# Kernel tuning notes

Hardware: AMD Instinct MI355X
Metric: run time of the kernel (lower is better)

The kernel has to match this reference:

```python
import jax, jax.numpy as jnp
import numpy as np

B, F, H, D, K = 16384, 4096, 512, 64, 512  # batch, feat, hidden, emb_dim, codebook size
M = H // D  # code positions per sample


def _leaky(h):
    return jnp.where(h > 0, h, 0.01 * h)


def setup_inputs() -> dict:
    key = jax.random.key(0)
    ks = jax.random.split(key, 16)
    lin = lambda k, i, o: jax.random.normal(k, (i, o), jnp.float32) * (1.0 / np.sqrt(i))
    return {
        "x": jax.random.uniform(ks[0], (B, F), jnp.float32),
        "We1": lin(ks[1], F, 256), "be1": jnp.zeros((256,), jnp.float32),
        "We2": lin(ks[2], 256, 128), "be2": jnp.zeros((128,), jnp.float32),
        "We3": lin(ks[3], 128, H), "be3": jnp.zeros((H,), jnp.float32),
        "Wd1": lin(ks[4], H, 128), "bd1": jnp.zeros((128,), jnp.float32),
        "Wd2": lin(ks[5], 128, 256), "bd2": jnp.zeros((256,), jnp.float32),
        "Wd3": lin(ks[6], 256, F), "bd3": jnp.zeros((F,), jnp.float32),
        "codebook": jax.random.normal(ks[7], (D, K), jnp.float32) * 0.02,  # (emb_dim, num_embeddings)
    }


def _nearest(z_e, codebook):
    # z_e: (B, D, M); codebook: (D, K). Squared-distance argmin over K.
    x2 = jnp.sum(z_e * z_e, axis=1)                       # (B, M)
    xw = jnp.einsum('bdm,dk->bmk', z_e, codebook)         # (B, M, K)
    w2 = jnp.sum(codebook * codebook, axis=0)             # (K,)
    idx = jnp.argmin(x2[..., None] - 2.0 * xw + w2, axis=-1)  # (B, M)
    quant = jnp.swapaxes(codebook.T[idx], 1, 2)           # (B, D, M)
    return quant, idx


def reference(x, We1, be1, We2, be2, We3, be3, Wd1, bd1, Wd2, bd2, Wd3, bd3, codebook):
    # encoder MLP
    h = _leaky(x @ We1 + be1)
    h = _leaky(h @ We2 + be2)
    h = _leaky(h @ We3 + be3)                             # (B, H)
    z_e = h.reshape(B, D, M)
    # emb(z_e, weight_sg=True): straight-through, weight detached
    quant_sg, idx = _nearest(z_e, jax.lax.stop_gradient(codebook))
    z_q = z_e + jax.lax.stop_gradient(quant_sg - z_e)
    # emb(z_e.detach()): grads (if any) flow to codebook via gather
    emb, _ = _nearest(jax.lax.stop_gradient(z_e), codebook)
    # decoder MLP
    g = _leaky(z_q.reshape(B, H) @ Wd1 + bd1)
    g = _leaky(g @ Wd2 + bd2)
    X_pred = jax.nn.sigmoid(g @ Wd3 + bd3)                # (B, F)
    return idx, z_e, z_q, emb, X_pred
```

## Files before the change

kernel.cpp:

```cpp
#include <hip/hip_runtime.h>
#include <cstdint>
#include <cstddef>


static constexpr int BB = 16384;

typedef __attribute__((ext_vector_type(8))) short short8;
typedef __attribute__((ext_vector_type(8))) _Float16 half8;
typedef __attribute__((ext_vector_type(4))) float f32x4;

__device__ __forceinline__ unsigned short f2bf(float f) {
    union { float f; uint32_t u; } v; v.f = f;
    uint32_t r = (v.u + 0x7FFFu + ((v.u >> 16) & 1u)) >> 16;
    return (unsigned short)r;
}

__device__ __forceinline__ void lds_barrier() {
    asm volatile("s_waitcnt lgkmcnt(0)" ::: "memory");
    __builtin_amdgcn_s_barrier();
    __builtin_amdgcn_sched_barrier(0);
}

__global__ __launch_bounds__(256) void combine_act(
    const float* __restrict__ part, int S, size_t MN,
    const float* __restrict__ bias, int N,
    float* __restrict__ outF)
{
    const size_t e = ((size_t)blockIdx.x * 256 + threadIdx.x) * 4;
    if (e >= MN) return;
    float4 s = *(const float4*)(part + e);
    for (int i = 1; i < S; i++) {
        const float4 p = *(const float4*)(part + (size_t)i * MN + e);
        s.x += p.x; s.y += p.y; s.z += p.z; s.w += p.w;
    }
    const int col = (int)(e & (size_t)(N - 1));
    const float4 bv = *(const float4*)(bias + col);
    float v0 = s.x + bv.x, v1 = s.y + bv.y, v2 = s.z + bv.z, v3 = s.w + bv.w;
    v0 = (v0 > 0.f) ? v0 : 0.01f * v0;
    v1 = (v1 > 0.f) ? v1 : 0.01f * v1;
    v2 = (v2 > 0.f) ? v2 : 0.01f * v2;
    v3 = (v3 > 0.f) ? v3 : 0.01f * v3;
    float4 o; o.x = v0; o.y = v1; o.z = v2; o.w = v3;
    *(float4*)(outF + e) = o;
}

__global__ __launch_bounds__(256) void transpose_cast(
    const float* __restrict__ W, unsigned short* __restrict__ WT, int R, int Cc)
{
    __shared__ float s[32][33];
    const int tx = threadIdx.x & 31, ty = threadIdx.x >> 5;
    const int c0 = blockIdx.x * 32, r0 = blockIdx.y * 32;
#pragma unroll
    for (int i = 0; i < 4; i++)
        s[ty + i * 8][tx] = W[(size_t)(r0 + ty + i * 8) * Cc + c0 + tx];
    __syncthreads();
#pragma unroll
    for (int i = 0; i < 4; i++)
        WT[(size_t)(c0 + ty + i * 8) * R + r0 + tx] = f2bf(s[tx][ty + i * 8]);
}

__global__ __launch_bounds__(256) void transpose_split_f16(
    const float* __restrict__ W, unsigned short* __restrict__ Th,
    unsigned short* __restrict__ Tl, int R, int Cc)
{
    __shared__ float s[32][33];
    const int tx = threadIdx.x & 31, ty = threadIdx.x >> 5;
    const int c0 = blockIdx.x * 32, r0 = blockIdx.y * 32;
#pragma unroll
    for (int i = 0; i < 4; i++)
        s[ty + i * 8][tx] = W[(size_t)(r0 + ty + i * 8) * Cc + c0 + tx];
    __syncthreads();
#pragma unroll
    for (int i = 0; i < 4; i++) {
        const float f = s[tx][ty + i * 8];
        const _Float16 h = (_Float16)f;
        const float fh = (float)h;
        const _Float16 lo = (_Float16)((f - fh) * 4096.0f);
        union { _Float16 hf; unsigned short u; } ch, cl;
        ch.hf = h; cl.hf = lo;
        Th[(size_t)(c0 + ty + i * 8) * R + r0 + tx] = ch.u;
        Tl[(size_t)(c0 + ty + i * 8) * R + r0 + tx] = cl.u;
    }
}

__global__ __launch_bounds__(512) void cb_w2(
    const float* __restrict__ cb, float* __restrict__ w2g)
{
    const int k = threadIdx.x;
    float s = 0.f;
    for (int d = 0; d < 64; d++) { float c = cb[d * 512 + k]; s = fmaf(c, c, s); }
    w2g[k] = s;
}

template<int BUF>
__device__ __forceinline__ void enc1_step(
    int K0,
    const float* __restrict__ gA,
    const unsigned short* __restrict__ gBh,
    const unsigned short* __restrict__ gBl,
    short (&Ah)[2][2048], short (&Al)[2][2048],
    half8 (&bhC)[4], half8 (&bhN)[4], half8 (&blS)[4],
    f32x4& p0, f32x4& p1,
    f32x4 (&acc1)[4][4], f32x4 (&acc2)[4][4],
    int aoff, int fr0)
{
    constexpr size_t rstep = (size_t)16 * 4096;
    const int kn1 = K0 + 32, kn2 = K0 + 64;
    lds_barrier();
#pragma unroll
    for (int j = 0; j < 4; j++)
        blS[j] = *(const half8*)(gBl + (size_t)j * rstep + K0);
    if (kn1 < 2048) {
#pragma unroll
        for (int j = 0; j < 4; j++)
            bhN[j] = *(const half8*)(gBh + (size_t)j * rstep + kn1);
    }
    f32x4 f0, f1;
    if (kn2 < 2048) {
        f0 = __builtin_nontemporal_load((const f32x4*)(gA + kn2));
        f1 = __builtin_nontemporal_load((const f32x4*)(gA + kn2 + 4));
    }
    half8 ah[4];
#pragma unroll
    for (int i = 0; i < 4; i++)
        ah[i] = *(const half8*)&Ah[BUF][(i << 9) + fr0];
#pragma unroll
    for (int i = 0; i < 4; i++)
#pragma unroll
        for (int j = 0; j < 4; j++)
            acc1[i][j] = __builtin_amdgcn_mfma_f32_16x16x32_f16(
                ah[i], bhC[j], acc1[i][j], 0, 0, 0);
#pragma unroll
    for (int i = 0; i < 4; i++)
#pragma unroll
        for (int j = 0; j < 4; j++)
            acc2[i][j] = __builtin_amdgcn_mfma_f32_16x16x32_f16(
                ah[i], blS[j], acc2[i][j], 0, 0, 0);
    half8 al[4];
#pragma unroll
    for (int i = 0; i < 4; i++)
        al[i] = *(const half8*)&Al[BUF][(i << 9) + fr0];
#pragma unroll
    for (int i = 0; i < 4; i++)
#pragma unroll
        for (int j = 0; j < 4; j++)
            acc2[i][j] = __builtin_amdgcn_mfma_f32_16x16x32_f16(
                al[i], bhC[j], acc2[i][j], 0, 0, 0);
    if (kn1 < 2048) {
        float fv[8];
        *(f32x4*)&fv[0] = p0;
        *(f32x4*)&fv[4] = p1;
        union { _Float16 h[8]; short8 s; } uh, ul;
#pragma unroll
        for (int e = 0; e < 8; e++) {
            const float f = fv[e];
            const _Float16 h = (_Float16)f;
            const float fh = (float)h;
            uh.h[e] = h;
            ul.h[e] = (_Float16)((f - fh) * 4096.0f);
        }
        *(short8*)&Ah[BUF ^ 1][aoff] = uh.s;
        *(short8*)&Al[BUF ^ 1][aoff] = ul.s;
    }
    if (kn2 < 2048) { p0 = f0; p1 = f1; }
}

__global__ __launch_bounds__(256, 2) void gemm_f16x2_enc1(
    const float* __restrict__ X,
    const unsigned short* __restrict__ Bh,
    const unsigned short* __restrict__ Bl,
    float* __restrict__ part)
{
    __shared__ short Ah[2][2048];
    __shared__ short Al[2][2048];
    const int tid = threadIdx.x;
    const int l = tid & 63, w = tid >> 6;
    const int lm = l & 15, lq = l >> 4;
    const int bm = blockIdx.y * 64;
    const int kStart = blockIdx.z * 2048;

    const float* gA = X + (size_t)(bm + w * 16 + lm) * 4096 + kStart + lq * 8;
    const unsigned short* gBh = Bh + (size_t)(w * 64 + lm) * 4096 + kStart + lq * 8;
    const unsigned short* gBl = Bl + (size_t)(w * 64 + lm) * 4096 + kStart + lq * 8;
    constexpr size_t rstep = (size_t)16 * 4096;

    const int aoff = (w << 9) + (l << 3);
    const int fr0 = (lq << 7) + (lm << 3);

    f32x4 acc1[4][4], acc2[4][4];
#pragma unroll
    for (int i = 0; i < 4; i++)
#pragma unroll
        for (int j = 0; j < 4; j++) {
            acc1[i][j] = (f32x4){0.f, 0.f, 0.f, 0.f};
            acc2[i][j] = (f32x4){0.f, 0.f, 0.f, 0.f};
        }

    half8 bhA[4], bhB[4], blS[4];
    f32x4 p0, p1;

    {
#pragma unroll
        for (int j = 0; j < 4; j++)
            bhA[j] = *(const half8*)(gBh + (size_t)j * rstep);
        f32x4 a0 = __builtin_nontemporal_load((const f32x4*)(gA));
        f32x4 a1 = __builtin_nontemporal_load((const f32x4*)(gA + 4));
        p0 = __builtin_nontemporal_load((const f32x4*)(gA + 32));
        p1 = __builtin_nontemporal_load((const f32x4*)(gA + 36));
        float fv[8];
        *(f32x4*)&fv[0] = a0;
        *(f32x4*)&fv[4] = a1;
        union { _Float16 h[8]; short8 s; } uh, ul;
#pragma unroll
        for (int e = 0; e < 8; e++) {
            const float f = fv[e];
            const _Float16 h = (_Float16)f;
            const float fh = (float)h;
            uh.h[e] = h;
            ul.h[e] = (_Float16)((f - fh) * 4096.0f);
        }
        *(short8*)&Ah[0][aoff] = uh.s;
        *(short8*)&Al[0][aoff] = ul.s;
    }

    for (int k2 = 0; k2 < 2048; k2 += 64) {
        enc1_step<0>(k2,      gA, gBh, gBl, Ah, Al, bhA, bhB, blS,
                     p0, p1, acc1, acc2, aoff, fr0);
        enc1_step<1>(k2 + 32, gA, gBh, gBl, Ah, Al, bhB, bhA, blS,
                     p0, p1, acc1, acc2, aoff, fr0);
    }

    float* P = part + (size_t)blockIdx.z * BB * 256;
    const float inv = 0.000244140625f;
#pragma unroll
    for (int i = 0; i < 4; i++)
#pragma unroll
        for (int j = 0; j < 4; j++) {
            const int col = w * 64 + j * 16 + lm;
#pragma unroll
            for (int r = 0; r < 4; r++) {
                const int row = bm + i * 16 + lq * 4 + r;
                P[(size_t)row * 256 + col] = acc1[i][j][r] + inv * acc2[i][j][r];
            }
        }
}

template<int BUF, int NJ, int KLEN>
__device__ __forceinline__ void mid_step(
    int K0,
    const float* __restrict__ gA,
    const unsigned short* __restrict__ gBh,
    const unsigned short* __restrict__ gBl,
    short (&Ah)[2][2048], short (&Al)[2][2048],
    half8 (&bhC)[NJ], half8 (&bhN)[NJ], half8 (&blS)[NJ],
    f32x4& p0, f32x4& p1,
    f32x4 (&acc1)[4][NJ], f32x4 (&acc2)[4][NJ],
    int aoff, int fr0)
{
    constexpr size_t rstep = (size_t)16 * KLEN;
    const int kn1 = K0 + 32, kn2 = K0 + 64;
    lds_barrier();
#pragma unroll
    for (int j = 0; j < NJ; j++)
        blS[j] = *(const half8*)(gBl + (size_t)j * rstep + K0);
    if (kn1 < KLEN) {
#pragma unroll
        for (int j = 0; j < NJ; j++)
            bhN[j] = *(const half8*)(gBh + (size_t)j * rstep + kn1);
    }
    f32x4 f0, f1;
    if (kn2 < KLEN) {
        f0 = *(const f32x4*)(gA + kn2);
        f1 = *(const f32x4*)(gA + kn2 + 4);
    }
    half8 ah[4];
#pragma unroll
    for (int i = 0; i < 4; i++)
        ah[i] = *(const half8*)&Ah[BUF][(i << 9) + fr0];
#pragma unroll
    for (int i = 0; i < 4; i++)
#pragma unroll
        for (int j = 0; j < NJ; j++)
            acc1[i][j] = __builtin_amdgcn_mfma_f32_16x16x32_f16(
                ah[i], bhC[j], acc1[i][j], 0, 0, 0);
#pragma unroll
    for (int i = 0; i < 4; i++)
#pragma unroll
        for (int j = 0; j < NJ; j++)
            acc2[i][j] = __builtin_amdgcn_mfma_f32_16x16x32_f16(
                ah[i], blS[j], acc2[i][j], 0, 0, 0);
    half8 al[4];
#pragma unroll
    for (int i = 0; i < 4; i++)
        al[i] = *(const half8*)&Al[BUF][(i << 9) + fr0];
#pragma unroll
    for (int i = 0; i < 4; i++)
#pragma unroll
        for (int j = 0; j < NJ; j++)
            acc2[i][j] = __builtin_amdgcn_mfma_f32_16x16x32_f16(
                al[i], bhC[j], acc2[i][j], 0, 0, 0);
    if (kn1 < KLEN) {
        float fv[8];
        *(f32x4*)&fv[0] = p0;
        *(f32x4*)&fv[4] = p1;
        union { _Float16 h[8]; short8 s; } uh, ul;
#pragma unroll
        for (int e = 0; e < 8; e++) {
            const float f = fv[e];
            const _Float16 h = (_Float16)f;
            const float fh = (float)h;
            uh.h[e] = h;
            ul.h[e] = (_Float16)((f - fh) * 4096.0f);
        }
        *(short8*)&Ah[BUF ^ 1][aoff] = uh.s;
        *(short8*)&Al[BUF ^ 1][aoff] = ul.s;
    }
    if (kn2 < KLEN) { p0 = f0; p1 = f1; }
}

template<int NJ, int KLEN, int ACT>
__global__ __launch_bounds__(256, 2) void gemm_f16x2_mid(
    const float* __restrict__ A,
    const unsigned short* __restrict__ Bh,
    const unsigned short* __restrict__ Bl,
    const float* __restrict__ bias,
    float* __restrict__ Cf, unsigned short* __restrict__ Cb)
{
    __shared__ short Ah[2][2048];
    __shared__ short Al[2][2048];
    const int tid = threadIdx.x;
    const int l = tid & 63, w = tid >> 6;
    const int lm = l & 15, lq = l >> 4;
    const int bm = blockIdx.y * 64;
    const int bn = blockIdx.x * (64 * NJ);
    const int N = gridDim.x * 64 * NJ;

    const float* gA = A + (size_t)(bm + w * 16 + lm) * KLEN + lq * 8;
    const unsigned short* gBh = Bh + (size_t)(bn + w * (16 * NJ) + lm) * KLEN + lq * 8;
    const unsigned short* gBl = Bl + (size_t)(bn + w * (16 * NJ) + lm) * KLEN + lq * 8;
    constexpr size_t rstep = (size_t)16 * KLEN;

    const int aoff = (w << 9) + (l << 3);
    const int fr0 = (lq << 7) + (lm << 3);

    f32x4 acc1[4][NJ], acc2[4][NJ];
#pragma unroll
    for (int i = 0; i < 4; i++)
#pragma unroll
        for (int j = 0; j < NJ; j++) {
            acc1[i][j] = (f32x4){0.f, 0.f, 0.f, 0.f};
            acc2[i][j] = (f32x4){0.f, 0.f, 0.f, 0.f};
        }

    half8 bhA[NJ], bhB[NJ], blS[NJ];
    f32x4 p0, p1;

    {
#pragma unroll
        for (int j = 0; j < NJ; j++)
            bhA[j] = *(const half8*)(gBh + (size_t)j * rstep);
        f32x4 a0 = *(const f32x4*)(gA);
        f32x4 a1 = *(const f32x4*)(gA + 4);
        p0 = *(const f32x4*)(gA + 32);
        p1 = *(const f32x4*)(gA + 36);
        float fv[8];
        *(f32x4*)&fv[0] = a0;
        *(f32x4*)&fv[4] = a1;
        union { _Float16 h[8]; short8 s; } uh, ul;
#pragma unroll
        for (int e = 0; e < 8; e++) {
            const float f = fv[e];
            const _Float16 h = (_Float16)f;
            const float fh = (float)h;
            uh.h[e] = h;
            ul.h[e] = (_Float16)((f - fh) * 4096.0f);
        }
        *(short8*)&Ah[0][aoff] = uh.s;
        *(short8*)&Al[0][aoff] = ul.s;
    }

    for (int k2 = 0; k2 < KLEN; k2 += 64) {
        mid_step<0, NJ, KLEN>(k2,      gA, gBh, gBl, Ah, Al, bhA, bhB, blS,
                              p0, p1, acc1, acc2, aoff, fr0);
        mid_step<1, NJ, KLEN>(k2 + 32, gA, gBh, gBl, Ah, Al, bhB, bhA, blS,
                              p0, p1, acc1, acc2, aoff, fr0);
    }

    const float inv = 0.000244140625f;
#pragma unroll
    for (int i = 0; i < 4; i++)
#pragma unroll
        for (int j = 0; j < NJ; j++) {
            const int col = bn + w * (16 * NJ) + j * 16 + lm;
            const float bv = bias[col];
#pragma unroll
            for (int r = 0; r < 4; r++) {
                const int row = bm + i * 16 + lq * 4 + r;
                float v = acc1[i][j][r] + inv * acc2[i][j][r] + bv;
                v = (v > 0.f) ? v : 0.01f * v;
                if (ACT == 0) Cf[(size_t)row * N + col] = v;
                else          Cb[(size_t)row * N + col] = f2bf(v);
            }
        }
}

__device__ __forceinline__ void dec3_step(
    int kn,
    const unsigned short* __restrict__ gA,
    const unsigned short* __restrict__ gB,
    short8 (&afC)[4], short8 (&bfC)[4],
    short8 (&afN)[4], short8 (&bfN)[4],
    f32x4 (&acc)[4][4])
{
    if (kn < 256) {
#pragma unroll
        for (int i = 0; i < 4; i++)
            afN[i] = *(const short8*)(gA + (size_t)i * 16 * 256 + kn);
#pragma unroll
        for (int j = 0; j < 4; j++)
            bfN[j] = *(const short8*)(gB + (size_t)j * 16 * 256 + kn);
    }
#pragma unroll
    for (int i = 0; i < 4; i++)
#pragma unroll
        for (int j = 0; j < 4; j++)
            acc[i][j] = __builtin_amdgcn_mfma_f32_16x16x32_bf16(
                afC[i], bfC[j], acc[i][j], 0, 0, 0);
}

__global__ __launch_bounds__(256) void gemm_bf16_dec3(
    const unsigned short* __restrict__ Ag,
    const unsigned short* __restrict__ Bt,
    const float* __restrict__ bias, float* __restrict__ C)
{
    const int tid = threadIdx.x;
    const int l = tid & 63, w = tid >> 6;
    const int lm = l & 15, lq = l >> 4;
    const int bm = blockIdx.y * 128, bn = blockIdx.x * 128;
    const int wm = (w >> 1) * 64, wn = (w & 1) * 64;

    const unsigned short* gA = Ag + (size_t)(bm + wm + lm) * 256 + lq * 8;
    const unsigned short* gB = Bt + (size_t)(bn + wn + lm) * 256 + lq * 8;

    f32x4 acc[4][4];
#pragma unroll
    for (int i = 0; i < 4; i++)
#pragma unroll
        for (int j = 0; j < 4; j++) acc[i][j] = (f32x4){0.f, 0.f, 0.f, 0.f};

    short8 afA[4], afB[4], bfA[4], bfB[4];
#pragma unroll
    for (int i = 0; i < 4; i++)
        afA[i] = *(const short8*)(gA + (size_t)i * 16 * 256);
#pragma unroll
    for (int j = 0; j < 4; j++)
        bfA[j] = *(const short8*)(gB + (size_t)j * 16 * 256);

    for (int k0 = 0; k0 < 256; k0 += 64) {
        dec3_step(k0 + 32, gA, gB, afA, bfA, afB, bfB, acc);
        dec3_step(k0 + 64, gA, gB, afB, bfB, afA, bfA, acc);
    }

#pragma unroll
    for (int i = 0; i < 4; i++) {
#pragma unroll
        for (int j = 0; j < 4; j++) {
            const int col = bn + wn + j * 16 + lm;
            const float bv = bias[col];
#pragma unroll
            for (int r = 0; r < 4; r++) {
                const int row = bm + wm + i * 16 + lq * 4 + r;
                float v = acc[i][j][r] + bv;
                v = 1.0f / (1.0f + __expf(-v));
                C[(size_t)row * 4096 + col] = v;
            }
        }
    }
}

__global__ __launch_bounds__(256) void vq_mfma(
    const float* __restrict__ ze, const float* __restrict__ cb,
    const unsigned short* __restrict__ cbTh,
    const unsigned short* __restrict__ cbTl,
    const float* __restrict__ w2g,
    float* __restrict__ idxf, float* __restrict__ zq, float* __restrict__ emb)
{
    __shared__ short Ahh[2048], All[2048];
    __shared__ float As[64][33];
    __shared__ float redv[32][4];
    __shared__ int   redk[32][4];
    __shared__ int   kq[32];
    const int tid = threadIdx.x;
    const int l = tid & 63, w = tid >> 6;
    const int lm = l & 15, lq = l >> 4;
    const int b0 = blockIdx.x * 4;

    const unsigned short* gBh = cbTh + (size_t)(w * 128 + lm) * 64 + lq * 8;
    const unsigned short* gBl = cbTl + (size_t)(w * 128 + lm) * 64 + lq * 8;
    half8 bh[8], bl[8];
#pragma unroll
    for (int j = 0; j < 8; j++) {
        bh[j] = *(const half8*)(gBh + (size_t)j * 1024);
        bl[j] = *(const half8*)(gBl + (size_t)j * 1024);
    }

#pragma unroll
    for (int ff = 0; ff < 2; ff++) {
        const int e = (tid + ff * 256) * 4;
        const int s = e >> 9, r = e & 511, d = r >> 3, m = r & 7;
        const f32x4 v = *(const f32x4*)(ze + (size_t)b0 * 512 + e);
#pragma unroll
        for (int c = 0; c < 4; c++) {
            const float fv = v[c];
            const int row = s * 8 + m + c;
            As[d][row] = fv;
            const _Float16 h = (_Float16)fv;
            const float fh = (float)h;
            const _Float16 lo = (_Float16)((fv - fh) * 4096.0f);
            union { _Float16 hf; unsigned short u; } ch, cl;
            ch.hf = h; cl.hf = lo;
            const int off = (row >> 4) * 1024 + (d >> 5) * 512 +
                            ((d >> 3) & 3) * 128 + (row & 15) * 8 + (d & 7);
            Ahh[off] = (short)ch.u;
            All[off] = (short)cl.u;
        }
    }
    __syncthreads();

    f32x4 acc1[2][8], acc2[2][8];
#pragma unroll
    for (int i = 0; i < 2; i++)
#pragma unroll
        for (int j = 0; j < 8; j++) {
            acc1[i][j] = (f32x4){0.f, 0.f, 0.f, 0.f};
            acc2[i][j] = (f32x4){0.f, 0.f, 0.f, 0.f};
        }

    const int fr0 = lq * 128 + lm * 8;
    half8 ah0[2], al0[2];
#pragma unroll
    for (int i = 0; i < 2; i++) {
        ah0[i] = *(const half8*)&Ahh[i * 1024 + fr0];
        al0[i] = *(const half8*)&All[i * 1024 + fr0];
    }
#pragma unroll
    for (int i = 0; i < 2; i++)
#pragma unroll
        for (int j = 0; j < 8; j++)
            acc1[i][j] = __builtin_amdgcn_mfma_f32_16x16x32_f16(
                ah0[i], bh[j], acc1[i][j], 0, 0, 0);
#pragma unroll
    for (int i = 0; i < 2; i++)
#pragma unroll
        for (int j = 0; j < 8; j++)
            acc2[i][j] = __builtin_amdgcn_mfma_f32_16x16x32_f16(
                al0[i], bh[j], acc2[i][j], 0, 0, 0);
#pragma unroll
    for (int j = 0; j < 8; j++) {
        half8 nb = *(const half8*)(gBh + (size_t)j * 1024 + 32);
#pragma unroll
        for (int i = 0; i < 2; i++)
            acc2[i][j] = __builtin_amdgcn_mfma_f32_16x16x32_f16(
                ah0[i], bl[j], acc2[i][j], 0, 0, 0);
        bh[j] = nb;
    }
#pragma unroll
    for (int j = 0; j < 8; j++)
        bl[j] = *(const half8*)(gBl + (size_t)j * 1024 + 32);
    half8 ah1[2], al1[2];
#pragma unroll
    for (int i = 0; i < 2; i++) {
        ah1[i] = *(const half8*)&Ahh[i * 1024 + 512 + fr0];
        al1[i] = *(const half8*)&All[i * 1024 + 512 + fr0];
    }
#pragma unroll
    for (int i = 0; i < 2; i++)
#pragma unroll
        for (int j = 0; j < 8; j++)
            acc1[i][j] = __builtin_amdgcn_mfma_f32_16x16x32_f16(
                ah1[i], bh[j], acc1[i][j], 0, 0, 0);
#pragma unroll
    for (int i = 0; i < 2; i++)
#pragma unroll
        for (int j = 0; j < 8; j++)
            acc2[i][j] = __builtin_amdgcn_mfma_f32_16x16x32_f16(
                ah1[i], bl[j], acc2[i][j], 0, 0, 0);
#pragma unroll
    for (int i = 0; i < 2; i++)
#pragma unroll
        for (int j = 0; j < 8; j++)
            acc2[i][j] = __builtin_amdgcn_mfma_f32_16x16x32_f16(
                al1[i], bh[j], acc2[i][j], 0, 0, 0);

    const float inv = 0.000244140625f;
    float w2v[8];
#pragma unroll
    for (int j = 0; j < 8; j++) w2v[j] = w2g[w * 128 + j * 16 + lm];

#pragma unroll
    for (int i = 0; i < 2; i++)
#pragma unroll
        for (int r = 0; r < 4; r++) {
            float bd = 3.4e38f; int bk = 1 << 30;
#pragma unroll
            for (int j = 0; j < 8; j++) {
                const float s = acc1[i][j][r] + inv * acc2[i][j][r];
                const float dsc = w2v[j] - 2.0f * s;
                const int kc = w * 128 + j * 16 + lm;
                if (dsc < bd || (dsc == bd && kc < bk)) { bd = dsc; bk = kc; }
            }
#pragma unroll
            for (int off = 1; off < 16; off <<= 1) {
                const float od = __shfl_xor(bd, off);
                const int   ok = __shfl_xor(bk, off);
                if (od < bd || (od == bd && ok < bk)) { bd = od; bk = ok; }
            }
            if (lm == 0) {
                const int row = i * 16 + lq * 4 + r;
                redv[row][w] = bd;
                redk[row][w] = bk;
            }
        }
    __syncthreads();

    if (tid < 32) {
        float bd = redv[tid][0]; int bk = redk[tid][0];
#pragma unroll
        for (int ww = 1; ww < 4; ww++) {
            const float od = redv[tid][ww];
            const int   ok = redk[tid][ww];
            if (od < bd || (od == bd && ok < bk)) { bd = od; bk = ok; }
        }
        idxf[(size_t)b0 * 8 + tid] = (float)bk;
        kq[tid] = bk;
    }
    __syncthreads();

    {
        const int ss = tid >> 6, dd = tid & 63;
        float zq8[8], em8[8];
#pragma unroll
        for (int mm = 0; mm < 8; mm++) {
            const int k = kq[ss * 8 + mm];
            const float q = cb[dd * 512 + k];
            const float z = As[dd][ss * 8 + mm];
            em8[mm] = q;
            zq8[mm] = z + (q - z);
        }
        float* zqp = zq + (size_t)(b0 + ss) * 512 + dd * 8;
        float* emp = emb + (size_t)(b0 + ss) * 512 + dd * 8;
        *(float4*)zqp = *(float4*)&zq8[0];
        *(float4*)(zqp + 4) = *(float4*)&zq8[4];
        *(float4*)emp = *(float4*)&em8[0];
        *(float4*)(emp + 4) = *(float4*)&em8[4];
    }
}

extern "C" void kernel_launch(void* const* d_in, const int* in_sizes, int n_in,
                              void* d_out, int out_size, void* d_ws, size_t ws_size,
                              hipStream_t stream)
{
    const float* x   = (const float*)d_in[0];
    const float* We1 = (const float*)d_in[1];
    const float* be1 = (const float*)d_in[2];
    const float* We2 = (const float*)d_in[3];
    const float* be2 = (const float*)d_in[4];
    const float* We3 = (const float*)d_in[5];
    const float* be3 = (const float*)d_in[6];
    const float* Wd1 = (const float*)d_in[7];
    const float* bd1 = (const float*)d_in[8];
    const float* Wd2 = (const float*)d_in[9];
    const float* bd2 = (const float*)d_in[10];
    const float* Wd3 = (const float*)d_in[11];
    const float* bd3 = (const float*)d_in[12];
    const float* cb  = (const float*)d_in[13];

    float* out   = (float*)d_out;
    float* o_idx = out;
    float* o_ze  = o_idx + 131072;
    float* o_zq  = o_ze + 8388608;
    float* o_emb = o_zq + 8388608;
    float* o_X   = o_emb + 8388608;

    float* h1 = (float*)d_ws;
    float* h2 = h1 + (size_t)BB * 256;
    float* g1 = h1;
    unsigned short* g2b = (unsigned short*)(h1 + (size_t)BB * 128);
    unsigned short* WT  = (unsigned short*)h2;

    unsigned short* Bth  = (unsigned short*)(o_X + 16777216);
    unsigned short* Btl  = Bth + 1048576;
    unsigned short* W2h  = Btl + 1048576;
    unsigned short* W2l  = W2h + 32768;
    unsigned short* W3h  = W2l + 32768;
    unsigned short* W3l  = W3h + 65536;
    unsigned short* Wd1h = W3l + 65536;
    unsigned short* Wd1l = Wd1h + 65536;
    unsigned short* Wd2h = Wd1l + 65536;
    unsigned short* Wd2l = Wd2h + 32768;
    unsigned short* cbTh = Wd2l + 32768;
    unsigned short* cbTl = cbTh + 32768;
    float*          w2g  = (float*)(cbTl + 32768);

    transpose_split_f16<<<dim3(8, 128), 256, 0, stream>>>(We1, Bth, Btl, 4096, 256);
    transpose_split_f16<<<dim3(4, 8),   256, 0, stream>>>(We2, W2h, W2l, 256, 128);
    transpose_split_f16<<<dim3(16, 4),  256, 0, stream>>>(We3, W3h, W3l, 128, 512);
    transpose_split_f16<<<dim3(4, 16),  256, 0, stream>>>(Wd1, Wd1h, Wd1l, 512, 128);
    transpose_split_f16<<<dim3(8, 4),   256, 0, stream>>>(Wd2, Wd2h, Wd2l, 128, 256);
    transpose_split_f16<<<dim3(16, 2),  256, 0, stream>>>(cb, cbTh, cbTl, 64, 512);
    cb_w2<<<dim3(1), dim3(512), 0, stream>>>(cb, w2g);

    gemm_f16x2_enc1<<<dim3(1, 256, 2), 256, 0, stream>>>(x, Bth, Btl, o_X);
    combine_act<<<4096, 256, 0, stream>>>(o_X, 2, (size_t)BB * 256, be1, 256, h1);
    gemm_f16x2_mid<2, 256, 0><<<dim3(1, 256), 256, 0, stream>>>(
        h1, W2h, W2l, be2, h2, nullptr);
    gemm_f16x2_mid<4, 128, 0><<<dim3(2, 256), 256, 0, stream>>>(
        h2, W3h, W3l, be3, o_ze, nullptr);

    transpose_cast<<<dim3(128, 8), 256, 0, stream>>>(Wd3, WT, 256, 4096);

    vq_mfma<<<dim3(4096), dim3(256), 0, stream>>>(
        o_ze, cb, cbTh, cbTl, w2g, o_idx, o_zq, o_emb);

    gemm_f16x2_mid<2, 512, 0><<<dim3(1, 256), 256, 0, stream>>>(
        o_zq, Wd1h, Wd1l, bd1, g1, nullptr);
    gemm_f16x2_mid<4, 128, 1><<<dim3(1, 256), 256, 0, stream>>>(
        g1, Wd2h, Wd2l, bd2, nullptr, g2b);
    gemm_bf16_dec3<<<dim3(32, 128), 256, 0, stream>>>(g2b, WT, bd3, o_X);
}
```

Measured before the change: 1.021 ms.

## Deepen encoder A-prefetch and split VQ codebook scoring into two chunks

The first encoder GEMM now prefetches activation rows two K-steps ahead instead of one, rotating through an extra register stage (q0/q1), so global load latency is better hidden behind MFMA work. The VQ kernel now processes its 128 codebook columns per wave as two 64-column chunks and keeps a running argmin across them. This halves the accumulator and B-fragment registers held live at once, which may allow higher occupancy. The cost is more registers in the encoder GEMM, which could hurt its 2-blocks-per-CU occupancy, and less load/compute overlap inside each VQ chunk.

```diff
diff --git a/kernel.cpp b/kernel.cpp
--- a/kernel.cpp
+++ b/kernel.cpp
@@ -100,12 +100,12 @@
     const unsigned short* __restrict__ gBl,
     short (&Ah)[2][2048], short (&Al)[2][2048],
     half8 (&bhC)[4], half8 (&bhN)[4], half8 (&blS)[4],
-    f32x4& p0, f32x4& p1,
+    f32x4& p0, f32x4& p1, f32x4& q0, f32x4& q1,
     f32x4 (&acc1)[4][4], f32x4 (&acc2)[4][4],
     int aoff, int fr0)
 {
     constexpr size_t rstep = (size_t)16 * 4096;
-    const int kn1 = K0 + 32, kn2 = K0 + 64;
+    const int kn1 = K0 + 32, kn3 = K0 + 96;
     lds_barrier();
 #pragma unroll
     for (int j = 0; j < 4; j++)
@@ -116,9 +116,9 @@
             bhN[j] = *(const half8*)(gBh + (size_t)j * rstep + kn1);
     }
     f32x4 f0, f1;
-    if (kn2 < 2048) {
-        f0 = __builtin_nontemporal_load((const f32x4*)(gA + kn2));
-        f1 = __builtin_nontemporal_load((const f32x4*)(gA + kn2 + 4));
+    if (kn3 < 2048) {
+        f0 = __builtin_nontemporal_load((const f32x4*)(gA + kn3));
+        f1 = __builtin_nontemporal_load((const f32x4*)(gA + kn3 + 4));
     }
     half8 ah[4];
 #pragma unroll
@@ -162,7 +162,8 @@
         *(short8*)&Ah[BUF ^ 1][aoff] = uh.s;
         *(short8*)&Al[BUF ^ 1][aoff] = ul.s;
     }
-    if (kn2 < 2048) { p0 = f0; p1 = f1; }
+    p0 = q0; p1 = q1;
+    if (kn3 < 2048) { q0 = f0; q1 = f1; }
 }
 
 __global__ __launch_bounds__(256, 2) void gemm_f16x2_enc1(
@@ -197,7 +198,7 @@
         }
 
     half8 bhA[4], bhB[4], blS[4];
-    f32x4 p0, p1;
+    f32x4 p0, p1, q0, q1;
 
     {
 #pragma unroll
@@ -207,6 +208,8 @@
         f32x4 a1 = __builtin_nontemporal_load((const f32x4*)(gA + 4));
         p0 = __builtin_nontemporal_load((const f32x4*)(gA + 32));
         p1 = __builtin_nontemporal_load((const f32x4*)(gA + 36));
+        q0 = __builtin_nontemporal_load((const f32x4*)(gA + 64));
+        q1 = __builtin_nontemporal_load((const f32x4*)(gA + 68));
         float fv[8];
         *(f32x4*)&fv[0] = a0;
         *(f32x4*)&fv[4] = a1;
@@ -225,9 +228,9 @@
 
     for (int k2 = 0; k2 < 2048; k2 += 64) {
         enc1_step<0>(k2,      gA, gBh, gBl, Ah, Al, bhA, bhB, blS,
-                     p0, p1, acc1, acc2, aoff, fr0);
+                     p0, p1, q0, q1, acc1, acc2, aoff, fr0);
         enc1_step<1>(k2 + 32, gA, gBh, gBl, Ah, Al, bhB, bhA, blS,
-                     p0, p1, acc1, acc2, aoff, fr0);
+                     p0, p1, q0, q1, acc1, acc2, aoff, fr0);
     }
 
     float* P = part + (size_t)blockIdx.z * BB * 256;
@@ -478,6 +481,98 @@
     }
 }
 
+template<int CH>
+__device__ __forceinline__ void vq_chunk(
+    int w, int lm, int lq, int fr0,
+    const short* Ahh, const short* All,
+    const unsigned short* __restrict__ cbTh,
+    const unsigned short* __restrict__ cbTl,
+    const float* __restrict__ w2g,
+    float (&bdv)[2][4], int (&bkv)[2][4])
+{
+    const unsigned short* gBh = cbTh + (size_t)(w * 128 + CH * 64 + lm) * 64 + lq * 8;
+    const unsigned short* gBl = cbTl + (size_t)(w * 128 + CH * 64 + lm) * 64 + lq * 8;
+    half8 bh0[4], bl0[4], bh1[4], bl1[4];
+#pragma unroll
+    for (int j = 0; j < 4; j++) {
+        bh0[j] = *(const half8*)(gBh + (size_t)j * 1024);
+        bl0[j] = *(const half8*)(gBl + (size_t)j * 1024);
+        bh1[j] = *(const half8*)(gBh + (size_t)j * 1024 + 32);
+        bl1[j] = *(const half8*)(gBl + (size_t)j * 1024 + 32);
+    }
+    half8 ah0[2], al0[2], ah1[2], al1[2];
+#pragma unroll
+    for (int i = 0; i < 2; i++) {
+        ah0[i] = *(const half8*)&Ahh[i * 1024 + fr0];
+        al0[i] = *(const half8*)&All[i * 1024 + fr0];
+        ah1[i] = *(const half8*)&Ahh[i * 1024 + 512 + fr0];
+        al1[i] = *(const half8*)&All[i * 1024 + 512 + fr0];
+    }
+    f32x4 acc1[2][4], acc2[2][4];
+#pragma unroll
+    for (int i = 0; i < 2; i++)
+#pragma unroll
+        for (int j = 0; j < 4; j++) {
+            acc1[i][j] = (f32x4){0.f, 0.f, 0.f, 0.f};
+            acc2[i][j] = (f32x4){0.f, 0.f, 0.f, 0.f};
+        }
+#pragma unroll
+    for (int i = 0; i < 2; i++)
+#pragma unroll
+        for (int j = 0; j < 4; j++)
+            acc1[i][j] = __builtin_amdgcn_mfma_f32_16x16x32_f16(
+                ah0[i], bh0[j], acc1[i][j], 0, 0, 0);
+#pragma unroll
+    for (int i = 0; i < 2; i++)
+#pragma unroll
+        for (int j = 0; j < 4; j++)
+            acc2[i][j] = __builtin_amdgcn_mfma_f32_16x16x32_f16(
+                al0[i], bh0[j], acc2[i][j], 0, 0, 0);
+#pragma unroll
+    for (int i = 0; i < 2; i++)
+#pragma unroll
+        for (int j = 0; j < 4; j++)
+            acc2[i][j] = __builtin_amdgcn_mfma_f32_16x16x32_f16(
+                ah0[i], bl0[j], acc2[i][j], 0, 0, 0);
+#pragma unroll
+    for (int i = 0; i < 2; i++)
+#pragma unroll
+        for (int j = 0; j < 4; j++)
+            acc1[i][j] = __builtin_amdgcn_mfma_f32_16x16x32_f16(
+                ah1[i], bh1[j], acc1[i][j], 0, 0, 0);
+#pragma unroll
+    for (int i = 0; i < 2; i++)
+#pragma unroll
+        for (int j = 0; j < 4; j++)
+            acc2[i][j] = __builtin_amdgcn_mfma_f32_16x16x32_f16(
+                ah1[i], bl1[j], acc2[i][j], 0, 0, 0);
+#pragma unroll
+    for (int i = 0; i < 2; i++)
+#pragma unroll
+        for (int j = 0; j < 4; j++)
+            acc2[i][j] = __builtin_amdgcn_mfma_f32_16x16x32_f16(
+                al1[i], bh1[j], acc2[i][j], 0, 0, 0);
+
+    const float inv = 0.000244140625f;
+    float w2v[4];
+#pragma unroll
+    for (int j = 0; j < 4; j++) w2v[j] = w2g[w * 128 + CH * 64 + j * 16 + lm];
+#pragma unroll
+    for (int i = 0; i < 2; i++)
+#pragma unroll
+        for (int r = 0; r < 4; r++) {
+            float bd = bdv[i][r]; int bk = bkv[i][r];
+#pragma unroll
+            for (int j = 0; j < 4; j++) {
+                const float s = acc1[i][j][r] + inv * acc2[i][j][r];
+                const float dsc = w2v[j] - 2.0f * s;
+                const int kc = w * 128 + CH * 64 + j * 16 + lm;
+                if (dsc < bd || (dsc == bd && kc < bk)) { bd = dsc; bk = kc; }
+            }
+            bdv[i][r] = bd; bkv[i][r] = bk;
+        }
+}
+
 __global__ __launch_bounds__(256) void vq_mfma(
     const float* __restrict__ ze, const float* __restrict__ cb,
     const unsigned short* __restrict__ cbTh,
@@ -494,15 +589,6 @@
     const int l = tid & 63, w = tid >> 6;
     const int lm = l & 15, lq = l >> 4;
     const int b0 = blockIdx.x * 4;
-
-    const unsigned short* gBh = cbTh + (size_t)(w * 128 + lm) * 64 + lq * 8;
-    const unsigned short* gBl = cbTl + (size_t)(w * 128 + lm) * 64 + lq * 8;
-    half8 bh[8], bl[8];
-#pragma unroll
-    for (int j = 0; j < 8; j++) {
-        bh[j] = *(const half8*)(gBh + (size_t)j * 1024);
-        bl[j] = *(const half8*)(gBl + (size_t)j * 1024);
-    }
 
 #pragma unroll
     for (int ff = 0; ff < 2; ff++) {
@@ -527,88 +613,22 @@
     }
     __syncthreads();
 
-    f32x4 acc1[2][8], acc2[2][8];
-#pragma unroll
-    for (int i = 0; i < 2; i++)
-#pragma unroll
-        for (int j = 0; j < 8; j++) {
-            acc1[i][j] = (f32x4){0.f, 0.f, 0.f, 0.f};
-            acc2[i][j] = (f32x4){0.f, 0.f, 0.f, 0.f};
-        }
-
     const int fr0 = lq * 128 + lm * 8;
-    half8 ah0[2], al0[2];
-#pragma unroll
-    for (int i = 0; i < 2; i++) {
-        ah0[i] = *(const half8*)&Ahh[i * 1024 + fr0];
-        al0[i] = *(const half8*)&All[i * 1024 + fr0];
-    }
-#pragma unroll
-    for (int i = 0; i < 2; i++)
-#pragma unroll
-        for (int j = 0; j < 8; j++)
-            acc1[i][j] = __builtin_amdgcn_mfma_f32_16x16x32_f16(
-                ah0[i], bh[j], acc1[i][j], 0, 0, 0);
-#pragma unroll
-    for (int i = 0; i < 2; i++)
-#pragma unroll
-        for (int j = 0; j < 8; j++)
-            acc2[i][j] = __builtin_amdgcn_mfma_f32_16x16x32_f16(
-                al0[i], bh[j], acc2[i][j], 0, 0, 0);
-#pragma unroll
-    for (int j = 0; j < 8; j++) {
-        half8 nb = *(const half8*)(gBh + (size_t)j * 1024 + 32);
-#pragma unroll
-        for (int i = 0; i < 2; i++)
-            acc2[i][j] = __builtin_amdgcn_mfma_f32_16x16x32_f16(
-                ah0[i], bl[j], acc2[i][j], 0, 0, 0);
-        bh[j] = nb;
-    }
-#pragma unroll
-    for (int j = 0; j < 8; j++)
-        bl[j] = *(const half8*)(gBl + (size_t)j * 1024 + 32);
-    half8 ah1[2], al1[2];
-#pragma unroll
-    for (int i = 0; i < 2; i++) {
-        ah1[i] = *(const half8*)&Ahh[i * 1024 + 512 + fr0];
-        al1[i] = *(const half8*)&All[i * 1024 + 512 + fr0];
-    }
-#pragma unroll
-    for (int i = 0; i < 2; i++)
-#pragma unroll
-        for (int j = 0; j < 8; j++)
-            acc1[i][j] = __builtin_amdgcn_mfma_f32_16x16x32_f16(
-                ah1[i], bh[j], acc1[i][j], 0, 0, 0);
-#pragma unroll
-    for (int i = 0; i < 2; i++)
-#pragma unroll
-        for (int j = 0; j < 8; j++)
-            acc2[i][j] = __builtin_amdgcn_mfma_f32_16x16x32_f16(
-                ah1[i], bl[j], acc2[i][j], 0, 0, 0);
-#pragma unroll
-    for (int i = 0; i < 2; i++)
-#pragma unroll
-        for (int j = 0; j < 8; j++)
-            acc2[i][j] = __builtin_amdgcn_mfma_f32_16x16x32_f16(
-                al1[i], bh[j], acc2[i][j], 0, 0, 0);
-
-    const float inv = 0.000244140625f;
-    float w2v[8];
-#pragma unroll
-    for (int j = 0; j < 8; j++) w2v[j] = w2g[w * 128 + j * 16 + lm];
+    float bdv[2][4];
+    int   bkv[2][4];
+#pragma unroll
+    for (int i = 0; i < 2; i++)
+#pragma unroll
+        for (int r = 0; r < 4; r++) { bdv[i][r] = 3.4e38f; bkv[i][r] = 1 << 30; }
+
+    vq_chunk<0>(w, lm, lq, fr0, Ahh, All, cbTh, cbTl, w2g, bdv, bkv);
+    vq_chunk<1>(w, lm, lq, fr0, Ahh, All, cbTh, cbTl, w2g, bdv, bkv);
 
 #pragma unroll
     for (int i = 0; i < 2; i++)
 #pragma unroll
         for (int r = 0; r < 4; r++) {
-            float bd = 3.4e38f; int bk = 1 << 30;
-#pragma unroll
-            for (int j = 0; j < 8; j++) {
-                const float s = acc1[i][j][r] + inv * acc2[i][j][r];
-                const float dsc = w2v[j] - 2.0f * s;
-                const int kc = w * 128 + j * 16 + lm;
-                if (dsc < bd || (dsc == bd && kc < bk)) { bd = dsc; bk = kc; }
-            }
+            float bd = bdv[i][r]; int bk = bkv[i][r];
 #pragma unroll
             for (int off = 1; off < 16; off <<= 1) {
                 const float od = __shfl_xor(bd, off);
```

Result: faster. 966.0 us (-5.4%).
